# Kernel tuning notes

Measured on AMD Instinct MI355X. Metric: run time of the kernel, lower is better.

Reference implementation:

```python
import jax, jax.numpy as jnp
import numpy as np

B, S, d, D = 128, 1024, 64, 64  # batch, seq_len, physical dim, bond dim


def setup_inputs() -> dict:
    key = jax.random.key(0)
    k1, k2, k3, k4 = jax.random.split(key, 4)
    k_core = (d * D * D) ** (-0.5)
    k_vec = d ** (-0.5)
    core = k_core * jax.random.normal(k1, (d, D, D), dtype=jnp.float32)
    left_boundary = k_vec * jax.random.normal(k2, (D,), dtype=jnp.float32)
    right_boundary = k_vec * jax.random.normal(k3, (D,), dtype=jnp.float32)
    X = jax.random.randint(k4, (B, S), 0, d, dtype=jnp.int32)
    return {"X": X, "core": core, "left_boundary": left_boundary,
            "right_boundary": right_boundary}


def reference(X, core, left_boundary, right_boundary):
    """Faithful JAX version of TTrain._log_contract_at_batch (homogeneous).

    X: [B, S] int category indices; core: [d, D, D]; boundaries: [D].
    Returns logprobs: [B].
    The per-step normalization (infinity-norm) + accumulated log-norm trick of
    the original is preserved exactly; the final
    log((exp(lognorm) * out)**2) is computed in the mathematically identical
    stable form 2*(lognorm + log|out|).
    """
    batch = X.shape[0]
    lb = jnp.broadcast_to(left_boundary, (batch, left_boundary.shape[0]))  # [B, D]
    Z0 = jnp.max(jnp.abs(lb), axis=1)                                      # [B]
    c0 = lb / Z0[:, None]
    logn0 = jnp.log(Z0)

    def step(carry, x_t):
        c, logn = carry                       # c: [B, D]
        w_t = core[x_t]                       # gather selected cores: [B, D, D]
        ct = jnp.einsum('bi,bij->bj', c, w_t)  # [B, D]
        Zt = jnp.max(jnp.abs(ct), axis=1)      # [B] infinity norm
        return (ct / Zt[:, None], logn + jnp.log(Zt)), None

    (c, logn), _ = jax.lax.scan(step, (c0, logn0), X.T)  # scan over seq axis
    out = jnp.einsum('bi,i->b', c, right_boundary)        # [B]
    logprobs = 2.0 * (logn + jnp.log(jnp.abs(out)))
    return logprobs
```

## Files before the change

kernel.cpp:

```cpp
#include <hip/hip_runtime.h>
#include <math.h>


#define TT_S 1024
#define TT_D 64
#define NCHUNK 16
#define CLEN 64

typedef __attribute__((ext_vector_type(8))) short short8;
typedef __attribute__((ext_vector_type(4))) float float4v;
typedef __attribute__((ext_vector_type(4))) unsigned uint4v;
typedef __attribute__((ext_vector_type(2))) unsigned uint2v;

static __device__ __forceinline__ short8 as_short8(uint4v u) {
    union { uint4v u; short8 s; } x; x.u = u; return x.s;
}

__global__ __launch_bounds__(256) void tt_prep(
    const float* __restrict__ core, short* __restrict__ tblA,
    short* __restrict__ tblBt)
{
    const int x = blockIdx.x;
    const int l = threadIdx.x & 63, r = threadIdx.x >> 6;
    const int n = l & 15, q = l >> 4;
    const float* W = core + x * 4096;

    if (r < 2) {
        #pragma unroll
        for (int Ii = 0; Ii < 2; ++Ii) {
            const int I = 2 * r + Ii;
            #pragma unroll
            for (int Kp = 0; Kp < 2; ++Kp) {
                short8 v;
                const int row = 16 * I + n;
                const int c0 = 32 * Kp + 4 * q;
                #pragma unroll
                for (int j = 0; j < 8; ++j) {
                    const int col = c0 + 16 * (j >> 2) + (j & 3);
                    v[j] = (short)(__float_as_uint(W[row * 64 + col]) >> 16);
                }
                *(short8*)(tblA + ((size_t)(x * 8 + I * 2 + Kp) * 64 + l) * 8) = v;
            }
        }
    } else {
        const int Kp = r - 2;
        #pragma unroll
        for (int J = 0; J < 4; ++J) {
            short8 v;
            const int col = 16 * J + n;
            const int r0 = 32 * Kp + 4 * q;
            #pragma unroll
            for (int j = 0; j < 8; ++j) {
                const int row = r0 + 16 * (j >> 2) + (j & 3);
                v[j] = (short)(__float_as_uint(W[row * 64 + col]) >> 16);
            }
            *(short8*)(tblBt + ((size_t)(x * 8 + Kp * 4 + J) * 64 + l) * 8) = v;
        }
    }
}

__global__ __launch_bounds__(64, 2) void tt_stage1(
    const int* __restrict__ X, const short* __restrict__ tblA,
    const short* __restrict__ tblBt, short* __restrict__ PT,
    float* __restrict__ ln1)
{
    const int w = blockIdx.x;
    const int b = w >> 4, chunk = w & 15;
    const int l = threadIdx.x, n = l & 15, q = l >> 4;

    const int xv = X[b * TT_S + chunk * CLEN + l];
    #define XT(t) __builtin_amdgcn_readlane(xv, (t))

    const float4v zero = {0.f, 0.f, 0.f, 0.f};
    float4v acc[4][4];
    short8 A0[8], A1[8];
    float logn = 0.f;

    #define PK(hi, lo) __builtin_amdgcn_perm(__float_as_uint(hi),             \
                                             __float_as_uint(lo), 0x07060302u)

    #define LOAD_FRAGS(DST, TBL, XIDX)                                        \
    {   const short8* p_ = (const short8*)((TBL) + (size_t)(XIDX) * 4096) + l; \
        _Pragma("unroll")                                                     \
        for (int f_ = 0; f_ < 8; ++f_) (DST)[f_] = p_[f_ * 64]; }

    #define MFMA_TBL(ABUF, BBUF)                                              \
        _Pragma("unroll")                                                     \
        for (int I_ = 0; I_ < 4; ++I_)                                        \
            _Pragma("unroll")                                                 \
            for (int J_ = 0; J_ < 4; ++J_) {                                  \
                float4v c0_ = __builtin_amdgcn_mfma_f32_16x16x32_bf16(        \
                    (ABUF)[2 * I_ + 0], (BBUF)[J_], zero, 0, 0, 0);           \
                acc[I_][J_] = __builtin_amdgcn_mfma_f32_16x16x32_bf16(        \
                    (ABUF)[2 * I_ + 1], (BBUF)[4 + J_], c0_, 0, 0, 0);        \
            }

    #define PROD(ABUF)                                                        \
        _Pragma("unroll")                                                     \
        for (int J_ = 0; J_ < 4; ++J_) {                                      \
            uint4v u0_, u1_;                                                  \
            u0_[0] = PK(acc[0][J_][1], acc[0][J_][0]);                        \
            u0_[1] = PK(acc[0][J_][3], acc[0][J_][2]);                        \
            u0_[2] = PK(acc[1][J_][1], acc[1][J_][0]);                        \
            u0_[3] = PK(acc[1][J_][3], acc[1][J_][2]);                        \
            u1_[0] = PK(acc[2][J_][1], acc[2][J_][0]);                        \
            u1_[1] = PK(acc[2][J_][3], acc[2][J_][2]);                        \
            u1_[2] = PK(acc[3][J_][1], acc[3][J_][0]);                        \
            u1_[3] = PK(acc[3][J_][3], acc[3][J_][2]);                        \
            const short8 bl_ = as_short8(u0_);                                \
            const short8 bh_ = as_short8(u1_);                                \
            _Pragma("unroll")                                                 \
            for (int I_ = 0; I_ < 4; ++I_) {                                  \
                float4v c0_ = __builtin_amdgcn_mfma_f32_16x16x32_bf16(        \
                    (ABUF)[2 * I_ + 0], bl_, zero, 0, 0, 0);                  \
                acc[I_][J_] = __builtin_amdgcn_mfma_f32_16x16x32_bf16(        \
                    (ABUF)[2 * I_ + 1], bh_, c0_, 0, 0, 0);                   \
            }                                                                 \
        }

    #define RENORM()                                                          \
    {   float Z_ = 0.f;                                                       \
        _Pragma("unroll")                                                     \
        for (int I_ = 0; I_ < 4; ++I_)                                        \
            _Pragma("unroll")                                                 \
            for (int J_ = 0; J_ < 4; ++J_)                                    \
                _Pragma("unroll")                                             \
                for (int r_ = 0; r_ < 4; ++r_)                                \
                    Z_ = fmaxf(Z_, fabsf(acc[I_][J_][r_]));                   \
        _Pragma("unroll")                                                     \
        for (int m_ = 32; m_; m_ >>= 1) Z_ = fmaxf(Z_, __shfl_xor(Z_, m_));   \
        logn += logf(Z_);                                                     \
        const float rZ_ = 1.0f / Z_;                                          \
        _Pragma("unroll")                                                     \
        for (int I_ = 0; I_ < 4; ++I_)                                        \
            _Pragma("unroll")                                                 \
            for (int J_ = 0; J_ < 4; ++J_)                                    \
                _Pragma("unroll")                                             \
                for (int r_ = 0; r_ < 4; ++r_) acc[I_][J_][r_] *= rZ_; }

    {
        short8 Bt[8];
        LOAD_FRAGS(Bt, tblBt, XT(CLEN - 1))
        LOAD_FRAGS(A0, tblA, XT(CLEN - 2))
        LOAD_FRAGS(A1, tblA, XT(CLEN - 3))
        MFMA_TBL(A0, Bt)
    }
    LOAD_FRAGS(A0, tblA, XT(CLEN - 4))

    #pragma unroll 1
    for (int it = 0; it < 31; ++it) {
        PROD(A1)
        {
            const int tn = 59 - 2 * it;
            LOAD_FRAGS(A1, tblA, XT(tn < 0 ? 0 : tn))
        }
        if (((2 * it + 2) & 7) == 0) RENORM()
        PROD(A0)
        {
            const int tn = 58 - 2 * it;
            LOAD_FRAGS(A0, tblA, XT(tn < 0 ? 0 : tn))
        }
    }

    {
        float Z = 0.f;
        #pragma unroll
        for (int I = 0; I < 4; ++I)
            #pragma unroll
            for (int J = 0; J < 4; ++J)
                #pragma unroll
                for (int r = 0; r < 4; ++r) Z = fmaxf(Z, fabsf(acc[I][J][r]));
        #pragma unroll
        for (int m = 32; m; m >>= 1) Z = fmaxf(Z, __shfl_xor(Z, m));
        logn += logf(Z);
        const float rZ = 1.0f / Z;
        short* base = PT + (size_t)w * 4096;
        #pragma unroll
        for (int I = 0; I < 4; ++I)
            #pragma unroll
            for (int J = 0; J < 4; ++J) {
                float4v v = acc[I][J];
                #pragma unroll
                for (int r = 0; r < 4; ++r) v[r] *= rZ;
                uint2v dd;
                dd[0] = PK(v[1], v[0]);
                dd[1] = PK(v[3], v[2]);
                *(uint2v*)(base + (16 * J + n) * 64 + 16 * I + 4 * q) = dd;
            }
        if (l == 0) ln1[w] = logn;
    }
    #undef LOAD_FRAGS
    #undef MFMA_TBL
    #undef PROD
    #undef RENORM
    #undef PK
    #undef XT
}

__global__ __launch_bounds__(64, 1) void tt_stage2(
    const short* __restrict__ PT, const float* __restrict__ ln1,
    const float* __restrict__ lb, const float* __restrict__ rb,
    float* __restrict__ out)
{
    __shared__ float cb[64];
    const int b = blockIdx.x, j = threadIdx.x;

    float c = lb[j];
    float Z = fabsf(c);
    #pragma unroll
    for (int m = 32; m; m >>= 1) Z = fmaxf(Z, __shfl_xor(Z, m));
    float logn = logf(Z);
    c *= (1.0f / Z);

    float ln = (j < NCHUNK) ? ln1[b * NCHUNK + j] : 0.f;
    #pragma unroll
    for (int m = 32; m; m >>= 1) ln += __shfl_xor(ln, m);
    logn += ln;

    const short* base = PT + (size_t)b * NCHUNK * 4096 + j * 64;

    short8 bufA[8], bufB[8];
    #pragma unroll
    for (int f = 0; f < 8; ++f) bufA[f] = ((const short8*)base)[f];

    #define S2_STEP(BUF)                                                      \
    {                                                                         \
        cb[j] = c;                                                            \
        asm volatile("s_waitcnt lgkmcnt(0)" ::: "memory");                    \
        float a0 = 0.f, a1 = 0.f, a2 = 0.f, a3 = 0.f;                         \
        _Pragma("unroll")                                                     \
        for (int f = 0; f < 8; ++f) {                                         \
            union { short8 s; uint4v u; } uu; uu.s = (BUF)[f];                \
            const float4v cv0 = *(const float4v*)(cb + 8 * f);                \
            const float4v cv1 = *(const float4v*)(cb + 8 * f + 4);            \
            a0 = fmaf(cv0[0], __uint_as_float(uu.u[0] << 16), a0);            \
            a1 = fmaf(cv0[1], __uint_as_float(uu.u[0] & 0xffff0000u), a1);    \
            a2 = fmaf(cv0[2], __uint_as_float(uu.u[1] << 16), a2);            \
            a3 = fmaf(cv0[3], __uint_as_float(uu.u[1] & 0xffff0000u), a3);    \
            a0 = fmaf(cv1[0], __uint_as_float(uu.u[2] << 16), a0);            \
            a1 = fmaf(cv1[1], __uint_as_float(uu.u[2] & 0xffff0000u), a1);    \
            a2 = fmaf(cv1[2], __uint_as_float(uu.u[3] << 16), a2);            \
            a3 = fmaf(cv1[3], __uint_as_float(uu.u[3] & 0xffff0000u), a3);    \
        }                                                                     \
        float cn = (a0 + a1) + (a2 + a3);                                     \
        float Zl = fabsf(cn);                                                 \
        _Pragma("unroll")                                                     \
        for (int m = 32; m; m >>= 1) Zl = fmaxf(Zl, __shfl_xor(Zl, m));       \
        logn += logf(Zl);                                                     \
        c = cn * (1.0f / Zl);                                                 \
    }

    #pragma unroll 1
    for (int k = 0; k < NCHUNK; k += 2) {
        {   const short8* p = (const short8*)(base + (size_t)(k + 1) * 4096);
            #pragma unroll
            for (int f = 0; f < 8; ++f) bufB[f] = p[f];
        }
        asm volatile("" ::: "memory");
        S2_STEP(bufA)
        {   const int kn = (k + 2 < NCHUNK) ? (k + 2) : (NCHUNK - 1);
            const short8* p = (const short8*)(base + (size_t)kn * 4096);
            #pragma unroll
            for (int f = 0; f < 8; ++f) bufA[f] = p[f];
        }
        asm volatile("" ::: "memory");
        S2_STEP(bufB)
    }
    #undef S2_STEP

    float dot = c * rb[j];
    #pragma unroll
    for (int m = 32; m; m >>= 1) dot += __shfl_xor(dot, m);
    if (j == 0) out[b] = 2.0f * (logn + logf(fabsf(dot)));
}

__global__ __launch_bounds__(256) void tt_transpose(
    const float* __restrict__ core, float* __restrict__ coreT)
{
    __shared__ float tile[64][65];
    const int x = blockIdx.x;
    const float* src = core + x * 4096;
    float* dst = coreT + x * 4096;
    const int r0 = threadIdx.x >> 6, cc = threadIdx.x & 63;
    #pragma unroll
    for (int k = 0; k < 16; ++k) tile[r0 + 4 * k][cc] = src[(r0 + 4 * k) * 64 + cc];
    __syncthreads();
    #pragma unroll
    for (int k = 0; k < 16; ++k) dst[(r0 + 4 * k) * 64 + cc] = tile[cc][r0 + 4 * k];
}

__global__ __launch_bounds__(64, 1) void ttrain_chain2(
    const int* __restrict__ X, const float* __restrict__ coreT,
    const float* __restrict__ lb, const float* __restrict__ rb,
    float* __restrict__ out)
{
    __shared__ float cbuf[2][64];
    const int b = blockIdx.x, j = threadIdx.x;
    const int* Xrow = X + b * TT_S;
    float c = lb[j];
    float Z = fabsf(c);
    #pragma unroll
    for (int m = 32; m; m >>= 1) Z = fmaxf(Z, __shfl_xor(Z, m));
    float logn = logf(Z);
    c *= (1.0f / Z);
    const float* colbase = coreT + j * 64;
    int xs_cur = Xrow[j];
    int xs_nxt = Xrow[64 + j];
    float4 wA[16], wB[16];
    {
        const int x0 = Xrow[0];
        const float4* p = (const float4*)(colbase + x0 * 4096);
        #pragma unroll
        for (int k = 0; k < 16; ++k) wA[k] = p[k];
    }
    #define TT_STEP(WCUR, WNXT, SLOT, XNEXT, T)                              \
    {                                                                        \
        cbuf[SLOT][j] = c;                                                   \
        {                                                                    \
            const float4* pre = (const float4*)(colbase + (XNEXT) * 4096);   \
            _Pragma("unroll")                                                \
            for (int k = 0; k < 16; ++k) WNXT[k] = pre[k];                   \
        }                                                                    \
        asm volatile("s_waitcnt lgkmcnt(0)" ::: "memory");                   \
        float a0 = 0.f, a1 = 0.f, a2 = 0.f, a3 = 0.f;                        \
        const float4* cb2 = (const float4*)cbuf[SLOT];                       \
        _Pragma("unroll")                                                    \
        for (int k = 0; k < 16; ++k) {                                       \
            float4 cv = cb2[k];                                              \
            a0 = fmaf(cv.x, WCUR[k].x, a0);                                  \
            a1 = fmaf(cv.y, WCUR[k].y, a1);                                  \
            a2 = fmaf(cv.z, WCUR[k].z, a2);                                  \
            a3 = fmaf(cv.w, WCUR[k].w, a3);                                  \
        }                                                                    \
        float cn = (a0 + a1) + (a2 + a3);                                    \
        if (((T) & 7) == 7) {                                                \
            float Zl = fabsf(cn);                                            \
            _Pragma("unroll")                                                \
            for (int m = 32; m; m >>= 1) Zl = fmaxf(Zl, __shfl_xor(Zl, m));  \
            logn += logf(Zl);                                                \
            cn *= (1.0f / Zl);                                               \
        }                                                                    \
        c = cn;                                                              \
    }
    for (int tc = 0; tc < TT_S; tc += 64) {
        #pragma unroll 1
        for (int u = 0; u < 64; u += 2) {
            const int x1 = __builtin_amdgcn_readlane(xs_cur, u + 1);
            TT_STEP(wA, wB, 0, x1, tc + u)
            const int src2 = (u + 2 < 64) ? xs_cur : xs_nxt;
            const int x2 = __builtin_amdgcn_readlane(src2, (u + 2) & 63);
            TT_STEP(wB, wA, 1, x2, tc + u + 1)
        }
        xs_cur = xs_nxt;
        const int nc = tc + 128;
        xs_nxt = Xrow[((nc < TT_S) ? nc : 0) + j];
    }
    #undef TT_STEP
    float dot = c * rb[j];
    #pragma unroll
    for (int m = 32; m; m >>= 1) dot += __shfl_xor(dot, m);
    if (j == 0) out[b] = 2.0f * (logn + logf(fabsf(dot)));
}

extern "C" void kernel_launch(void* const* d_in, const int* in_sizes, int n_in,
                              void* d_out, int out_size, void* d_ws, size_t ws_size,
                              hipStream_t stream) {
    const int*   X    = (const int*)d_in[0];
    const float* core = (const float*)d_in[1];
    const float* lb   = (const float*)d_in[2];
    const float* rb   = (const float*)d_in[3];
    float* out = (float*)d_out;

    const int B = in_sizes[0] / TT_S;
    const size_t tblBytes = (size_t)64 * 8 * 64 * 8 * sizeof(short);
    const size_t ptBytes  = (size_t)B * NCHUNK * 4096 * sizeof(short);
    const size_t lnBytes  = (size_t)B * NCHUNK * sizeof(float);
    const size_t need = 2 * tblBytes + ptBytes + lnBytes;

    if (ws_size >= need) {
        char* w = (char*)d_ws;
        short* tblA  = (short*)w;
        short* tblBt = (short*)(w + tblBytes);
        short* PT    = (short*)(w + 2 * tblBytes);
        float* ln1   = (float*)(w + 2 * tblBytes + ptBytes);
        tt_prep<<<64, 256, 0, stream>>>(core, tblA, tblBt);
        tt_stage1<<<B * NCHUNK, 64, 0, stream>>>(X, tblA, tblBt, PT, ln1);
        tt_stage2<<<B, 64, 0, stream>>>(PT, ln1, lb, rb, out);
    } else if (ws_size >= (size_t)64 * 4096 * sizeof(float)) {
        float* coreT = (float*)d_ws;
        tt_transpose<<<64, 256, 0, stream>>>(core, coreT);
        ttrain_chain2<<<B, TT_D, 0, stream>>>(X, coreT, lb, rb, out);
    }
}
```

Baseline: 137.6 us.

## Switch chunk matrix products from 16x16x32 to 32x32x16 bf16 MFMA tiles

Reorganizes the per-chunk 64x64 matrix chain products to use 32x32x16 bf16 MFMA instructions with 2x2 output tiles of 16 floats each, instead of 4x4 tiles of 16x16x32 MFMAs. The prep kernel's fragment tables, the accumulator-to-B-operand repacking, renormalization and the final store layout are all rewritten to match the 32x32 register layout. The aim is higher MFMA throughput per instruction and fewer instructions in the serial chain. In exchange each MFMA has longer latency and the chain per output tile is deeper (4 dependent MFMAs), which could hurt a latency-bound serial product.

```diff
diff --git a/kernel.cpp b/kernel.cpp
--- a/kernel.cpp
+++ b/kernel.cpp
@@ -9,6 +9,7 @@
 
 typedef __attribute__((ext_vector_type(8))) short short8;
 typedef __attribute__((ext_vector_type(4))) float float4v;
+typedef __attribute__((ext_vector_type(16))) float float16v;
 typedef __attribute__((ext_vector_type(4))) unsigned uint4v;
 typedef __attribute__((ext_vector_type(2))) unsigned uint2v;
 
@@ -22,40 +23,34 @@
 {
     const int x = blockIdx.x;
     const int l = threadIdx.x & 63, r = threadIdx.x >> 6;
-    const int n = l & 15, q = l >> 4;
+    const int nh = l & 31, h = l >> 5;
     const float* W = core + x * 4096;
 
-    if (r < 2) {
-        #pragma unroll
-        for (int Ii = 0; Ii < 2; ++Ii) {
-            const int I = 2 * r + Ii;
-            #pragma unroll
-            for (int Kp = 0; Kp < 2; ++Kp) {
-                short8 v;
-                const int row = 16 * I + n;
-                const int c0 = 32 * Kp + 4 * q;
-                #pragma unroll
-                for (int j = 0; j < 8; ++j) {
-                    const int col = c0 + 16 * (j >> 2) + (j & 3);
-                    v[j] = (short)(__float_as_uint(W[row * 64 + col]) >> 16);
-                }
-                *(short8*)(tblA + ((size_t)(x * 8 + I * 2 + Kp) * 64 + l) * 8) = v;
-            }
-        }
-    } else {
-        const int Kp = r - 2;
-        #pragma unroll
-        for (int J = 0; J < 4; ++J) {
-            short8 v;
-            const int col = 16 * J + n;
-            const int r0 = 32 * Kp + 4 * q;
+    #pragma unroll
+    for (int fi = 0; fi < 4; ++fi) {
+        const int f = 4 * r + fi;
+        short8 v;
+        short* dst;
+        if (f < 8) {
+            const int I = f >> 2, Kb = f & 3;
+            const int row = 32 * I + nh;
             #pragma unroll
             for (int j = 0; j < 8; ++j) {
-                const int row = r0 + 16 * (j >> 2) + (j & 3);
+                const int col = 16 * Kb + (j & 3) + 8 * (j >> 2) + 4 * h;
                 v[j] = (short)(__float_as_uint(W[row * 64 + col]) >> 16);
             }
-            *(short8*)(tblBt + ((size_t)(x * 8 + Kp * 4 + J) * 64 + l) * 8) = v;
-        }
+            dst = tblA + ((size_t)(x * 8 + f) * 64 + l) * 8;
+        } else {
+            const int fb = f - 8, Kb = fb >> 1, J = fb & 1;
+            const int col = 32 * J + nh;
+            #pragma unroll
+            for (int j = 0; j < 8; ++j) {
+                const int row = 16 * Kb + (j & 3) + 8 * (j >> 2) + 4 * h;
+                v[j] = (short)(__float_as_uint(W[row * 64 + col]) >> 16);
+            }
+            dst = tblBt + ((size_t)(x * 8 + fb) * 64 + l) * 8;
+        }
+        *(short8*)dst = v;
     }
 }
 
@@ -66,13 +61,13 @@
 {
     const int w = blockIdx.x;
     const int b = w >> 4, chunk = w & 15;
-    const int l = threadIdx.x, n = l & 15, q = l >> 4;
+    const int l = threadIdx.x, nh = l & 31, h = l >> 5;
 
     const int xv = X[b * TT_S + chunk * CLEN + l];
     #define XT(t) __builtin_amdgcn_readlane(xv, (t))
 
-    const float4v zero = {0.f, 0.f, 0.f, 0.f};
-    float4v acc[4][4];
+    const float16v zero16 = {0,0,0,0,0,0,0,0,0,0,0,0,0,0,0,0};
+    float16v acc[2][2];
     short8 A0[8], A1[8];
     float logn = 0.f;
 
@@ -86,57 +81,62 @@
 
     #define MFMA_TBL(ABUF, BBUF)                                              \
         _Pragma("unroll")                                                     \
-        for (int I_ = 0; I_ < 4; ++I_)                                        \
-            _Pragma("unroll")                                                 \
-            for (int J_ = 0; J_ < 4; ++J_) {                                  \
-                float4v c0_ = __builtin_amdgcn_mfma_f32_16x16x32_bf16(        \
-                    (ABUF)[2 * I_ + 0], (BBUF)[J_], zero, 0, 0, 0);           \
-                acc[I_][J_] = __builtin_amdgcn_mfma_f32_16x16x32_bf16(        \
-                    (ABUF)[2 * I_ + 1], (BBUF)[4 + J_], c0_, 0, 0, 0);        \
+        for (int I_ = 0; I_ < 2; ++I_)                                        \
+            _Pragma("unroll")                                                 \
+            for (int J_ = 0; J_ < 2; ++J_) {                                  \
+                float16v c_ = zero16;                                         \
+                _Pragma("unroll")                                             \
+                for (int Kb_ = 0; Kb_ < 4; ++Kb_)                             \
+                    c_ = __builtin_amdgcn_mfma_f32_32x32x16_bf16(             \
+                        (ABUF)[I_ * 4 + Kb_], (BBUF)[Kb_ * 2 + J_],           \
+                        c_, 0, 0, 0);                                         \
+                acc[I_][J_] = c_;                                             \
             }
 
     #define PROD(ABUF)                                                        \
         _Pragma("unroll")                                                     \
-        for (int J_ = 0; J_ < 4; ++J_) {                                      \
-            uint4v u0_, u1_;                                                  \
-            u0_[0] = PK(acc[0][J_][1], acc[0][J_][0]);                        \
-            u0_[1] = PK(acc[0][J_][3], acc[0][J_][2]);                        \
-            u0_[2] = PK(acc[1][J_][1], acc[1][J_][0]);                        \
-            u0_[3] = PK(acc[1][J_][3], acc[1][J_][2]);                        \
-            u1_[0] = PK(acc[2][J_][1], acc[2][J_][0]);                        \
-            u1_[1] = PK(acc[2][J_][3], acc[2][J_][2]);                        \
-            u1_[2] = PK(acc[3][J_][1], acc[3][J_][0]);                        \
-            u1_[3] = PK(acc[3][J_][3], acc[3][J_][2]);                        \
-            const short8 bl_ = as_short8(u0_);                                \
-            const short8 bh_ = as_short8(u1_);                                \
-            _Pragma("unroll")                                                 \
-            for (int I_ = 0; I_ < 4; ++I_) {                                  \
-                float4v c0_ = __builtin_amdgcn_mfma_f32_16x16x32_bf16(        \
-                    (ABUF)[2 * I_ + 0], bl_, zero, 0, 0, 0);                  \
-                acc[I_][J_] = __builtin_amdgcn_mfma_f32_16x16x32_bf16(        \
-                    (ABUF)[2 * I_ + 1], bh_, c0_, 0, 0, 0);                   \
+        for (int J_ = 0; J_ < 2; ++J_) {                                      \
+            short8 bb_[4];                                                    \
+            _Pragma("unroll")                                                 \
+            for (int Kb_ = 0; Kb_ < 4; ++Kb_) {                               \
+                const int I2_ = Kb_ >> 1, g_ = 8 * (Kb_ & 1);                 \
+                uint4v u_;                                                    \
+                u_[0] = PK(acc[I2_][J_][g_ + 1], acc[I2_][J_][g_ + 0]);       \
+                u_[1] = PK(acc[I2_][J_][g_ + 3], acc[I2_][J_][g_ + 2]);       \
+                u_[2] = PK(acc[I2_][J_][g_ + 5], acc[I2_][J_][g_ + 4]);       \
+                u_[3] = PK(acc[I2_][J_][g_ + 7], acc[I2_][J_][g_ + 6]);       \
+                bb_[Kb_] = as_short8(u_);                                     \
+            }                                                                 \
+            _Pragma("unroll")                                                 \
+            for (int I_ = 0; I_ < 2; ++I_) {                                  \
+                float16v c_ = zero16;                                         \
+                _Pragma("unroll")                                             \
+                for (int Kb_ = 0; Kb_ < 4; ++Kb_)                             \
+                    c_ = __builtin_amdgcn_mfma_f32_32x32x16_bf16(             \
+                        (ABUF)[I_ * 4 + Kb_], bb_[Kb_], c_, 0, 0, 0);         \
+                acc[I_][J_] = c_;                                             \
             }                                                                 \
         }
 
     #define RENORM()                                                          \
     {   float Z_ = 0.f;                                                       \
         _Pragma("unroll")                                                     \
-        for (int I_ = 0; I_ < 4; ++I_)                                        \
-            _Pragma("unroll")                                                 \
-            for (int J_ = 0; J_ < 4; ++J_)                                    \
+        for (int I_ = 0; I_ < 2; ++I_)                                        \
+            _Pragma("unroll")                                                 \
+            for (int J_ = 0; J_ < 2; ++J_)                                    \
                 _Pragma("unroll")                                             \
-                for (int r_ = 0; r_ < 4; ++r_)                                \
+                for (int r_ = 0; r_ < 16; ++r_)                               \
                     Z_ = fmaxf(Z_, fabsf(acc[I_][J_][r_]));                   \
         _Pragma("unroll")                                                     \
         for (int m_ = 32; m_; m_ >>= 1) Z_ = fmaxf(Z_, __shfl_xor(Z_, m_));   \
         logn += logf(Z_);                                                     \
         const float rZ_ = 1.0f / Z_;                                          \
         _Pragma("unroll")                                                     \
-        for (int I_ = 0; I_ < 4; ++I_)                                        \
-            _Pragma("unroll")                                                 \
-            for (int J_ = 0; J_ < 4; ++J_)                                    \
+        for (int I_ = 0; I_ < 2; ++I_)                                        \
+            _Pragma("unroll")                                                 \
+            for (int J_ = 0; J_ < 2; ++J_)                                    \
                 _Pragma("unroll")                                             \
-                for (int r_ = 0; r_ < 4; ++r_) acc[I_][J_][r_] *= rZ_; }
+                for (int r_ = 0; r_ < 16; ++r_) acc[I_][J_][r_] *= rZ_; }
 
     {
         short8 Bt[8];
@@ -165,27 +165,31 @@
     {
         float Z = 0.f;
         #pragma unroll
-        for (int I = 0; I < 4; ++I)
-            #pragma unroll
-            for (int J = 0; J < 4; ++J)
+        for (int I = 0; I < 2; ++I)
+            #pragma unroll
+            for (int J = 0; J < 2; ++J)
                 #pragma unroll
-                for (int r = 0; r < 4; ++r) Z = fmaxf(Z, fabsf(acc[I][J][r]));
+                for (int r = 0; r < 16; ++r) Z = fmaxf(Z, fabsf(acc[I][J][r]));
         #pragma unroll
         for (int m = 32; m; m >>= 1) Z = fmaxf(Z, __shfl_xor(Z, m));
         logn += logf(Z);
         const float rZ = 1.0f / Z;
         short* base = PT + (size_t)w * 4096;
         #pragma unroll
-        for (int I = 0; I < 4; ++I)
-            #pragma unroll
-            for (int J = 0; J < 4; ++J) {
-                float4v v = acc[I][J];
+        for (int I = 0; I < 2; ++I)
+            #pragma unroll
+            for (int J = 0; J < 2; ++J) {
+                float16v v = acc[I][J];
                 #pragma unroll
-                for (int r = 0; r < 4; ++r) v[r] *= rZ;
-                uint2v dd;
-                dd[0] = PK(v[1], v[0]);
-                dd[1] = PK(v[3], v[2]);
-                *(uint2v*)(base + (16 * J + n) * 64 + 16 * I + 4 * q) = dd;
+                for (int r = 0; r < 16; ++r) v[r] *= rZ;
+                #pragma unroll
+                for (int rg = 0; rg < 4; ++rg) {
+                    uint2v dd;
+                    dd[0] = PK(v[4 * rg + 1], v[4 * rg + 0]);
+                    dd[1] = PK(v[4 * rg + 3], v[4 * rg + 2]);
+                    *(uint2v*)(base + (32 * J + nh) * 64 + 32 * I
+                               + 8 * rg + 4 * h) = dd;
+                }
             }
         if (l == 0) ln1[w] = logn;
     }
```

Result: no change. 139.9 us (+1.7%).

## Interleave two independent 32-step chains per wave in stage1 to hide MFMA latency

Applied to the files above, without the earlier changes.

Each stage1 wave now computes two independent chunk products of 32 steps each (P and Q halves of a 64-token window) instead of one 64-step chain, interleaving their MFMA sequences. The goal is to hide the dependent-MFMA latency of a single serial chain through instruction-level parallelism. The cost is doubled accumulator and fragment registers per wave, which may hurt occupancy. NCHUNK doubles to 32, so stage2 must combine twice as many partial products and the PT workspace doubles.

```diff
diff --git a/kernel.cpp b/kernel.cpp
--- a/kernel.cpp
+++ b/kernel.cpp
@@ -4,8 +4,8 @@
 
 #define TT_S 1024
 #define TT_D 64
-#define NCHUNK 16
-#define CLEN 64
+#define NCHUNK 32
+#define CLEN 32
 
 typedef __attribute__((ext_vector_type(8))) short short8;
 typedef __attribute__((ext_vector_type(4))) float float4v;
@@ -65,16 +65,17 @@
     float* __restrict__ ln1)
 {
     const int w = blockIdx.x;
-    const int b = w >> 4, chunk = w & 15;
+    const int b = w >> 4, v = w & 15;
     const int l = threadIdx.x, n = l & 15, q = l >> 4;
 
-    const int xv = X[b * TT_S + chunk * CLEN + l];
-    #define XT(t) __builtin_amdgcn_readlane(xv, (t))
+    const int xv = X[b * TT_S + v * 64 + l];
+    #define XTP(t) __builtin_amdgcn_readlane(xv, (t))
+    #define XTQ(t) __builtin_amdgcn_readlane(xv, 32 + (t))
 
     const float4v zero = {0.f, 0.f, 0.f, 0.f};
-    float4v acc[4][4];
-    short8 A0[8], A1[8];
-    float logn = 0.f;
+    float4v accP[4][4], accQ[4][4];
+    short8 AP[8], AQ[8];
+    float lognP = 0.f, lognQ = 0.f;
 
     #define PK(hi, lo) __builtin_amdgcn_perm(__float_as_uint(hi),             \
                                              __float_as_uint(lo), 0x07060302u)
@@ -84,41 +85,41 @@
         _Pragma("unroll")                                                     \
         for (int f_ = 0; f_ < 8; ++f_) (DST)[f_] = p_[f_ * 64]; }
 
-    #define MFMA_TBL(ABUF, BBUF)                                              \
+    #define MFMA_TBL(ACC, ABUF, BBUF)                                         \
         _Pragma("unroll")                                                     \
         for (int I_ = 0; I_ < 4; ++I_)                                        \
             _Pragma("unroll")                                                 \
             for (int J_ = 0; J_ < 4; ++J_) {                                  \
                 float4v c0_ = __builtin_amdgcn_mfma_f32_16x16x32_bf16(        \
                     (ABUF)[2 * I_ + 0], (BBUF)[J_], zero, 0, 0, 0);           \
-                acc[I_][J_] = __builtin_amdgcn_mfma_f32_16x16x32_bf16(        \
+                (ACC)[I_][J_] = __builtin_amdgcn_mfma_f32_16x16x32_bf16(      \
                     (ABUF)[2 * I_ + 1], (BBUF)[4 + J_], c0_, 0, 0, 0);        \
             }
 
-    #define PROD(ABUF)                                                        \
+    #define PROD(ACC, ABUF)                                                   \
         _Pragma("unroll")                                                     \
         for (int J_ = 0; J_ < 4; ++J_) {                                      \
             uint4v u0_, u1_;                                                  \
-            u0_[0] = PK(acc[0][J_][1], acc[0][J_][0]);                        \
-            u0_[1] = PK(acc[0][J_][3], acc[0][J_][2]);                        \
-            u0_[2] = PK(acc[1][J_][1], acc[1][J_][0]);                        \
-            u0_[3] = PK(acc[1][J_][3], acc[1][J_][2]);                        \
-            u1_[0] = PK(acc[2][J_][1], acc[2][J_][0]);                        \
-            u1_[1] = PK(acc[2][J_][3], acc[2][J_][2]);                        \
-            u1_[2] = PK(acc[3][J_][1], acc[3][J_][0]);                        \
-            u1_[3] = PK(acc[3][J_][3], acc[3][J_][2]);                        \
+            u0_[0] = PK((ACC)[0][J_][1], (ACC)[0][J_][0]);                    \
+            u0_[1] = PK((ACC)[0][J_][3], (ACC)[0][J_][2]);                    \
+            u0_[2] = PK((ACC)[1][J_][1], (ACC)[1][J_][0]);                    \
+            u0_[3] = PK((ACC)[1][J_][3], (ACC)[1][J_][2]);                    \
+            u1_[0] = PK((ACC)[2][J_][1], (ACC)[2][J_][0]);                    \
+            u1_[1] = PK((ACC)[2][J_][3], (ACC)[2][J_][2]);                    \
+            u1_[2] = PK((ACC)[3][J_][1], (ACC)[3][J_][0]);                    \
+            u1_[3] = PK((ACC)[3][J_][3], (ACC)[3][J_][2]);                    \
             const short8 bl_ = as_short8(u0_);                                \
             const short8 bh_ = as_short8(u1_);                                \
             _Pragma("unroll")                                                 \
             for (int I_ = 0; I_ < 4; ++I_) {                                  \
                 float4v c0_ = __builtin_amdgcn_mfma_f32_16x16x32_bf16(        \
                     (ABUF)[2 * I_ + 0], bl_, zero, 0, 0, 0);                  \
-                acc[I_][J_] = __builtin_amdgcn_mfma_f32_16x16x32_bf16(        \
+                (ACC)[I_][J_] = __builtin_amdgcn_mfma_f32_16x16x32_bf16(      \
                     (ABUF)[2 * I_ + 1], bh_, c0_, 0, 0, 0);                   \
             }                                                                 \
         }
 
-    #define RENORM()                                                          \
+    #define RENORM(ACC, LOGN)                                                 \
     {   float Z_ = 0.f;                                                       \
         _Pragma("unroll")                                                     \
         for (int I_ = 0; I_ < 4; ++I_)                                        \
@@ -126,75 +127,81 @@
             for (int J_ = 0; J_ < 4; ++J_)                                    \
                 _Pragma("unroll")                                             \
                 for (int r_ = 0; r_ < 4; ++r_)                                \
-                    Z_ = fmaxf(Z_, fabsf(acc[I_][J_][r_]));                   \
+                    Z_ = fmaxf(Z_, fabsf((ACC)[I_][J_][r_]));                 \
         _Pragma("unroll")                                                     \
         for (int m_ = 32; m_; m_ >>= 1) Z_ = fmaxf(Z_, __shfl_xor(Z_, m_));   \
-        logn += logf(Z_);                                                     \
+        (LOGN) += logf(Z_);                                                   \
         const float rZ_ = 1.0f / Z_;                                          \
         _Pragma("unroll")                                                     \
         for (int I_ = 0; I_ < 4; ++I_)                                        \
             _Pragma("unroll")                                                 \
             for (int J_ = 0; J_ < 4; ++J_)                                    \
                 _Pragma("unroll")                                             \
-                for (int r_ = 0; r_ < 4; ++r_) acc[I_][J_][r_] *= rZ_; }
+                for (int r_ = 0; r_ < 4; ++r_) (ACC)[I_][J_][r_] *= rZ_; }
 
     {
         short8 Bt[8];
-        LOAD_FRAGS(Bt, tblBt, XT(CLEN - 1))
-        LOAD_FRAGS(A0, tblA, XT(CLEN - 2))
-        LOAD_FRAGS(A1, tblA, XT(CLEN - 3))
-        MFMA_TBL(A0, Bt)
-    }
-    LOAD_FRAGS(A0, tblA, XT(CLEN - 4))
+        LOAD_FRAGS(Bt, tblBt, XTP(CLEN - 1))
+        LOAD_FRAGS(AP, tblA, XTP(CLEN - 2))
+        MFMA_TBL(accP, AP, Bt)
+        LOAD_FRAGS(Bt, tblBt, XTQ(CLEN - 1))
+        LOAD_FRAGS(AQ, tblA, XTQ(CLEN - 2))
+        MFMA_TBL(accQ, AQ, Bt)
+    }
+    LOAD_FRAGS(AP, tblA, XTP(CLEN - 3))
+    LOAD_FRAGS(AQ, tblA, XTQ(CLEN - 3))
 
     #pragma unroll 1
-    for (int it = 0; it < 31; ++it) {
-        PROD(A1)
-        {
-            const int tn = 59 - 2 * it;
-            LOAD_FRAGS(A1, tblA, XT(tn < 0 ? 0 : tn))
-        }
-        if (((2 * it + 2) & 7) == 0) RENORM()
-        PROD(A0)
-        {
-            const int tn = 58 - 2 * it;
-            LOAD_FRAGS(A0, tblA, XT(tn < 0 ? 0 : tn))
-        }
-    }
-
-    {
-        float Z = 0.f;
-        #pragma unroll
-        for (int I = 0; I < 4; ++I)
-            #pragma unroll
-            for (int J = 0; J < 4; ++J)
-                #pragma unroll
-                for (int r = 0; r < 4; ++r) Z = fmaxf(Z, fabsf(acc[I][J][r]));
-        #pragma unroll
-        for (int m = 32; m; m >>= 1) Z = fmaxf(Z, __shfl_xor(Z, m));
-        logn += logf(Z);
-        const float rZ = 1.0f / Z;
-        short* base = PT + (size_t)w * 4096;
-        #pragma unroll
-        for (int I = 0; I < 4; ++I)
-            #pragma unroll
-            for (int J = 0; J < 4; ++J) {
-                float4v v = acc[I][J];
-                #pragma unroll
-                for (int r = 0; r < 4; ++r) v[r] *= rZ;
-                uint2v dd;
-                dd[0] = PK(v[1], v[0]);
-                dd[1] = PK(v[3], v[2]);
-                *(uint2v*)(base + (16 * J + n) * 64 + 16 * I + 4 * q) = dd;
-            }
-        if (l == 0) ln1[w] = logn;
-    }
+    for (int s = 2; s < CLEN; ++s) {
+        const int tn = CLEN - 1 - (s + 1);
+        const int tnc = tn < 0 ? 0 : tn;
+        if ((s & 7) == 0) RENORM(accP, lognP)
+        PROD(accP, AP)
+        LOAD_FRAGS(AP, tblA, XTP(tnc))
+        if ((s & 7) == 0) RENORM(accQ, lognQ)
+        PROD(accQ, AQ)
+        LOAD_FRAGS(AQ, tblA, XTQ(tnc))
+    }
+
+    #define EPILOG(ACC, LOGN, CHUNK)                                          \
+    {   float Z_ = 0.f;                                                       \
+        _Pragma("unroll")                                                     \
+        for (int I_ = 0; I_ < 4; ++I_)                                        \
+            _Pragma("unroll")                                                 \
+            for (int J_ = 0; J_ < 4; ++J_)                                    \
+                _Pragma("unroll")                                             \
+                for (int r_ = 0; r_ < 4; ++r_)                                \
+                    Z_ = fmaxf(Z_, fabsf((ACC)[I_][J_][r_]));                 \
+        _Pragma("unroll")                                                     \
+        for (int m_ = 32; m_; m_ >>= 1) Z_ = fmaxf(Z_, __shfl_xor(Z_, m_));   \
+        (LOGN) += logf(Z_);                                                   \
+        const float rZ_ = 1.0f / Z_;                                          \
+        short* base_ = PT + ((size_t)(b * NCHUNK + (CHUNK))) * 4096;          \
+        _Pragma("unroll")                                                     \
+        for (int I_ = 0; I_ < 4; ++I_)                                        \
+            _Pragma("unroll")                                                 \
+            for (int J_ = 0; J_ < 4; ++J_) {                                  \
+                float4v v_ = (ACC)[I_][J_];                                   \
+                _Pragma("unroll")                                             \
+                for (int r_ = 0; r_ < 4; ++r_) v_[r_] *= rZ_;                 \
+                uint2v dd_;                                                   \
+                dd_[0] = PK(v_[1], v_[0]);                                    \
+                dd_[1] = PK(v_[3], v_[2]);                                    \
+                *(uint2v*)(base_ + (16 * J_ + n) * 64 + 16 * I_ + 4 * q) = dd_; \
+            }                                                                 \
+        if (l == 0) ln1[b * NCHUNK + (CHUNK)] = (LOGN); }
+
+    EPILOG(accP, lognP, 2 * v)
+    EPILOG(accQ, lognQ, 2 * v + 1)
+
     #undef LOAD_FRAGS
     #undef MFMA_TBL
     #undef PROD
     #undef RENORM
+    #undef EPILOG
     #undef PK
-    #undef XT
+    #undef XTP
+    #undef XTQ
 }
 
 __global__ __launch_bounds__(64, 1) void tt_stage2(
@@ -384,7 +391,7 @@
         short* PT    = (short*)(w + 2 * tblBytes);
         float* ln1   = (float*)(w + 2 * tblBytes + ptBytes);
         tt_prep<<<64, 256, 0, stream>>>(core, tblA, tblBt);
-        tt_stage1<<<B * NCHUNK, 64, 0, stream>>>(X, tblA, tblBt, PT, ln1);
+        tt_stage1<<<B * 16, 64, 0, stream>>>(X, tblA, tblBt, PT, ln1);
         tt_stage2<<<B, 64, 0, stream>>>(PT, ln1, lb, rb, out);
     } else if (ws_size >= (size_t)64 * 4096 * sizeof(float)) {
         float* coreT = (float*)d_ws;
```

Result: slower. 150.8 us (+9.6%).
